# Kernel optimization log

Measured on AMD Instinct MI355X. Metric: run time of the kernel, lower is better.

Reference implementation:

```python
import jax, jax.numpy as jnp
import numpy as np

N = 4096
CIN = 128
COUT = 128
J = 2
SLOPE = 0.2        # LeakyReLU negative slope (GAT-style)
NEG = -9.0e15      # mask fill value from the source
ATT = J * COUT     # att_slice


def _leaky(v):
    return jnp.where(v >= 0, v, SLOPE * v)


def setup_inputs() -> dict:
    key = jax.random.key(0)
    ks = jax.random.split(key, 12)
    x = jax.random.normal(ks[0], (N, CIN), dtype=jnp.float32)

    def sparse_op(k):
        kv, km = jax.random.split(k)
        vals = jax.random.normal(kv, (N, N), dtype=jnp.float32)
        mask = jax.random.uniform(km, (N, N)) < 0.05
        return jnp.where(mask, vals, 0.0)

    Lu = sparse_op(ks[1])
    Ld = sparse_op(ks[2])
    P = jax.random.normal(ks[3], (N, N), dtype=jnp.float32) * 0.01  # harmonic projector

    s = 1.0 / np.sqrt(CIN)
    Wi_w = jax.random.uniform(ks[4], (J, CIN, COUT), minval=-s, maxval=s)
    Wi_b = jax.random.uniform(ks[5], (J, COUT), minval=-s, maxval=s)
    Ws_w = jax.random.uniform(ks[6], (J, CIN, COUT), minval=-s, maxval=s)
    Ws_b = jax.random.uniform(ks[7], (J, COUT), minval=-s, maxval=s)
    Wh_w = jax.random.uniform(ks[8], (CIN, COUT), minval=-s, maxval=s)
    Wh_b = jax.random.uniform(ks[9], (COUT,), minval=-s, maxval=s)
    att_irr = jax.random.normal(ks[10], (2 * ATT, 1), dtype=jnp.float32) * 0.1
    att_sol = jax.random.normal(ks[11], (2 * ATT, 1), dtype=jnp.float32) * 0.1
    return {"x": x, "Lu": Lu, "Ld": Ld, "P": P,
            "Wi_w": Wi_w, "Wi_b": Wi_b, "Ws_w": Ws_w, "Ws_b": Ws_b,
            "Wh_w": Wh_w, "Wh_b": Wh_b, "att_irr": att_irr, "att_sol": att_sol}


def reference(x, Lu, Ld, P, Wi_w, Wi_b, Ws_w, Ws_b, Wh_w, Wh_b, att_irr, att_sol):
    n = x.shape[0]
    # concat_j W_irr[j](x) -> [N, J*COUT] (j-major matches torch.cat along dim=1)
    x_irr = (jnp.einsum('nc,jco->njo', x, Wi_w) + Wi_b[None]).reshape(n, ATT)
    x_sol = (jnp.einsum('nc,jco->njo', x, Ws_w) + Ws_b[None]).reshape(n, ATT)

    # GAT-style scores: E[i,j] = leaky(s1[i] + s2[j])
    E_irr = _leaky(x_irr @ att_irr[:ATT] + (x_irr @ att_irr[ATT:]).T)
    E_sol = _leaky(x_sol @ att_sol[:ATT] + (x_sol @ att_sol[ATT:]).T)
    E_irr = jnp.where(Ld != 0, E_irr, NEG)
    E_sol = jnp.where(Lu != 0, E_sol, NEG)
    alpha_irr = jax.nn.softmax(E_irr, axis=1)  # dropout: eval mode -> identity
    alpha_sol = jax.nn.softmax(E_sol, axis=1)

    z = (alpha_irr @ x) @ Wi_w[0] + Wi_b[0] + (alpha_sol @ x) @ Ws_w[0] + Ws_b[0]
    for p in range(1, J):  # Laplacian-power aggregation
        alpha_irr = alpha_irr @ Ld
        alpha_sol = alpha_sol @ Lu
        z = z + (alpha_irr @ x) @ Wi_w[p] + Wi_b[p]
        z = z + (alpha_sol @ x) @ Ws_w[p] + Ws_b[p]
    z = z + (P @ x) @ Wh_w + Wh_b
    return z
```

## Files before the change

### kernel.cpp

```cpp
#include <hip/hip_runtime.h>

#define NN 4096
#define SLOPE 0.2f

typedef float f4_t __attribute__((ext_vector_type(4)));
typedef __bf16 bf8v __attribute__((ext_vector_type(8)));
typedef float f32x16 __attribute__((ext_vector_type(16)));

#define V_OFF     0
#define C_OFF     512
#define BT_OFF    516
#define S_OFF     1024
#define DEN_OFF   20480
#define HXI_OFF   32768
#define HXS_OFF   (HXI_OFF + NN*128)
#define UI_OFF    (HXS_OFF + NN*128)
#define US_OFF    (UI_OFF + NN*128)
#define XWH_OFF   (US_OFF + NN*128)
#define OI_OFF    (XWH_OFF + NN*128)
#define OS_OFF    (OI_OFF + NN*128)
#define ZP_OFF    (OS_OFF + NN*128)
#define WS_FLOATS (ZP_OFF + 8*NN*128)
#define XF_BYTE_OFF ((size_t)WS_FLOATS * 4)

#define XI(c)   ((c) + (((c) >> 5) << 2))

#define FRAG(c, k) ((size_t)((k) >> 4) * 2048 + (size_t)((c) >> 5) * 512 \
                    + (size_t)((((c) & 31) + 32 * (((k) >> 3) & 1)) * 8 + ((k) & 7)))

__device__ __forceinline__ unsigned short f2bf(float x) {
  unsigned u = __float_as_uint(x);
  return (unsigned short)((u + 0x7FFFu + ((u >> 16) & 1u)) >> 16);
}
__device__ __forceinline__ float bf2f(unsigned short h) {
  return __uint_as_float(((unsigned)h) << 16);
}
union BFU { unsigned short u[8]; bf8v v; };

__global__ __launch_bounds__(128) void k_prep(
    const float* __restrict__ Wi_w, const float* __restrict__ Wi_b,
    const float* __restrict__ Ws_w, const float* __restrict__ Ws_b,
    const float* __restrict__ Wh_b, const float* __restrict__ att_irr,
    const float* __restrict__ att_sol, float* __restrict__ ws) {
  const int t = threadIdx.x;
  float v1i = 0.f, v2i = 0.f, v1s = 0.f, v2s = 0.f;
  for (int j = 0; j < 2; ++j) {
    for (int o = 0; o < 128; ++o) {
      const float wi = Wi_w[j*16384 + t*128 + o];
      const float wv = Ws_w[j*16384 + t*128 + o];
      v1i += wi * att_irr[j*128 + o];
      v2i += wi * att_irr[256 + j*128 + o];
      v1s += wv * att_sol[j*128 + o];
      v2s += wv * att_sol[256 + j*128 + o];
    }
  }
  ws[V_OFF + t]       = v1i;
  ws[V_OFF + 128 + t] = v2i;
  ws[V_OFF + 256 + t] = v1s;
  ws[V_OFF + 384 + t] = v2s;
  ws[BT_OFF + t] = Wi_b[t] + Wi_b[128 + t] + Ws_b[t] + Ws_b[128 + t] + Wh_b[t];
  if (t < 4) {
    const float* bb = (t < 2) ? Wi_b : Ws_b;
    const float* aa = ((t < 2) ? att_irr : att_sol) + ((t & 1) ? 256 : 0);
    float c = 0.f;
    for (int k = 0; k < 256; ++k) c += bb[k] * aa[k];
    ws[C_OFF + t] = c;
  }
}

__global__ __launch_bounds__(256) void k_zero(float* __restrict__ ws) {
  const size_t q = ((size_t)blockIdx.x * 256 + threadIdx.x) * 4;
  if (q < (size_t)2*NN*128) {
    *(f4_t*)&ws[HXI_OFF + q] = (f4_t){0.f, 0.f, 0.f, 0.f};
  } else if (q < (size_t)4*NN*128) {
    *(f4_t*)&ws[OI_OFF + (q - (size_t)2*NN*128)] = (f4_t){0.f, 0.f, 0.f, 0.f};
  } else {
    const size_t r = q - (size_t)4*NN*128;
    if (r < 2*NN) *(f4_t*)&ws[DEN_OFF + r] = (f4_t){0.f, 0.f, 0.f, 0.f};
  }
}

__global__ __launch_bounds__(256) void k_pre2(
    const float* __restrict__ x, const float* __restrict__ Wh_w,
    float* __restrict__ ws, unsigned short* __restrict__ xth,
    unsigned short* __restrict__ xtl, unsigned short* __restrict__ xfh,
    unsigned short* __restrict__ xfl) {
  __shared__ __align__(16) float At[32][33];
  __shared__ __align__(16) float Wt[32][144];
  const int t = threadIdx.x;

  if (blockIdx.x < 128) {
    const int rb = blockIdx.x;
    const int rg = t >> 4, cg = t & 15;
    const int r0 = rb * 32;
    float acc[2][8];
    #pragma unroll
    for (int i = 0; i < 2; ++i)
      #pragma unroll
      for (int j = 0; j < 8; ++j) acc[i][j] = 0.f;
    for (int k0 = 0; k0 < 128; k0 += 32) {
      __syncthreads();
      {
        const int row = t >> 3, kq = t & 7;
        const float4 av = *(const float4*)&x[(r0 + row)*128 + k0 + kq*4];
        At[row][kq*4+0] = av.x; At[row][kq*4+1] = av.y;
        At[row][kq*4+2] = av.z; At[row][kq*4+3] = av.w;
      }
      #pragma unroll
      for (int l = 0; l < 4; ++l) {
        const int idx = t + l*256;
        const int kr = idx >> 5, c4 = idx & 31;
        const float4 wv = *(const float4*)&Wh_w[(k0 + kr)*128 + c4*4];
        *(float4*)&Wt[kr][XI(c4*4)] = wv;
      }
      __syncthreads();
      #pragma unroll
      for (int k = 0; k < 32; ++k) {
        const float a0 = At[rg*2 + 0][k];
        const float a1 = At[rg*2 + 1][k];
        const float4 b0 = *(const float4*)&Wt[k][XI(cg*8)];
        const float4 b1 = *(const float4*)&Wt[k][XI(cg*8 + 4)];
        acc[0][0] += a0*b0.x; acc[0][1] += a0*b0.y; acc[0][2] += a0*b0.z; acc[0][3] += a0*b0.w;
        acc[0][4] += a0*b1.x; acc[0][5] += a0*b1.y; acc[0][6] += a0*b1.z; acc[0][7] += a0*b1.w;
        acc[1][0] += a1*b0.x; acc[1][1] += a1*b0.y; acc[1][2] += a1*b0.z; acc[1][3] += a1*b0.w;
        acc[1][4] += a1*b1.x; acc[1][5] += a1*b1.y; acc[1][6] += a1*b1.z; acc[1][7] += a1*b1.w;
      }
    }
    #pragma unroll
    for (int i = 0; i < 2; ++i) {
      const int r = r0 + rg*2 + i;
      #pragma unroll
      for (int j = 0; j < 8; ++j) {
        const int c = cg*8 + j;
        const float val = acc[i][j];
        const unsigned short h = f2bf(val);
        const unsigned short l = f2bf(val - bf2f(h));
        const size_t fa = FRAG(c, r);
        xth[fa] = h;
        xtl[fa] = l;
      }
    }
  } else {
    const int wave = t >> 6, lane = t & 63;
    const int row = (blockIdx.x - 128) * 4 + wave;
    const float* v = ws + V_OFF;
    const float x0 = x[row*128 + lane];
    const float x1 = x[row*128 + 64 + lane];
    {
      const unsigned short h0 = f2bf(x0);
      const unsigned short l0 = f2bf(x0 - bf2f(h0));
      const size_t fa0 = FRAG(lane, row);
      xfh[fa0] = h0; xfl[fa0] = l0;
      const unsigned short h1 = f2bf(x1);
      const unsigned short l1 = f2bf(x1 - bf2f(h1));
      const size_t fa1 = FRAG(lane + 64, row);
      xfh[fa1] = h1; xfl[fa1] = l1;
    }
    float p0 = x0 * v[lane]       + x1 * v[64 + lane];
    float p1 = x0 * v[128 + lane] + x1 * v[192 + lane];
    float p2 = x0 * v[256 + lane] + x1 * v[320 + lane];
    float p3 = x0 * v[384 + lane] + x1 * v[448 + lane];
    #pragma unroll
    for (int off = 32; off; off >>= 1) {
      p0 += __shfl_down(p0, off);
      p1 += __shfl_down(p1, off);
      p2 += __shfl_down(p2, off);
      p3 += __shfl_down(p3, off);
    }
    if (lane == 0) {
      ws[S_OFF + row]          = p0 + ws[C_OFF + 0];
      ws[S_OFF + NN + row]     = p1 + ws[C_OFF + 1];
      ws[S_OFF + 2*NN + row]   = p2 + ws[C_OFF + 2];
      ws[S_OFF + 3*NN + row]   = p3 + ws[C_OFF + 3];
    }
  }
}

__global__ __launch_bounds__(256) void k_hxmm(
    const float* __restrict__ Ld, const float* __restrict__ Lu,
    const unsigned short* __restrict__ xfh, const unsigned short* __restrict__ xfl,
    float* __restrict__ ws) {
  const int bid = blockIdx.x;
  const int br  = (bid >> 2) & 1;
  const int idx = ((bid >> 3) << 2) | (bid & 3);
  const int rblk = idx & 127;
  const int kz   = idx >> 7;
  const int t = threadIdx.x;
  const int w = t >> 6, lane = t & 63;
  const int la = lane & 31, h = lane >> 5;
  const int r0 = rblk * 32;
  const int kc = kz * 1024;
  const float* __restrict__ L = br ? Lu : Ld;
  float* __restrict__ Hx = ws + (br ? HXS_OFF : HXI_OFF);

  __shared__ __align__(16) char buf[2][16384];

  f32x16 acc;
  #pragma unroll
  for (int e = 0; e < 16; ++e) acc[e] = 0.f;

  const int col4 = la;
  const unsigned short* __restrict__ bh0 = xfh + ((size_t)kc >> 4) * 2048 + w * 512 + lane * 8;
  const unsigned short* __restrict__ bl0 = xfl + ((size_t)kc >> 4) * 2048 + w * 512 + lane * 8;

  f4_t rv[4];
  #pragma unroll
  for (int i = 0; i < 4; ++i) {
    const int row = w*8 + i*2 + h;
    rv[i] = *(const f4_t*)&L[(size_t)(r0 + row) * NN + kc + col4 * 4];
  }

  for (int tt = 0; tt < 8; ++tt) {
    char* bd = buf[tt & 1];
    #pragma unroll
    for (int i = 0; i < 4; ++i) {
      const int row = w*8 + i*2 + h;
      *(f4_t*)(bd + row*512 + ((col4*16) ^ ((row & 15) << 4))) = rv[i];
    }
    __syncthreads();
    if (tt + 1 < 8) {
      const int kcol = kc + (tt + 1) * 128;
      #pragma unroll
      for (int i = 0; i < 4; ++i) {
        const int row = w*8 + i*2 + h;
        rv[i] = *(const f4_t*)&L[(size_t)(r0 + row) * NN + kcol + col4 * 4];
      }
    }
    const char* tb = buf[tt & 1];
    const int rowb = la * 512;
    const int mask = (la & 15) << 4;
    #pragma unroll
    for (int s = 0; s < 8; ++s) {
      const int k0 = s * 16;
      const int b0 = k0 * 4 + 32 * h;
      const f4_t a0 = *(const f4_t*)(tb + rowb + ((b0) ^ mask));
      const f4_t a1 = *(const f4_t*)(tb + rowb + ((b0 + 16) ^ mask));
      BFU ah, al;
      #pragma unroll
      for (int i = 0; i < 8; ++i) {
        const float f = (i < 4) ? a0[i] : a1[i - 4];
        const unsigned short hh = f2bf(f);
        ah.u[i] = hh;
        al.u[i] = f2bf(f - bf2f(hh));
      }
      const size_t bo = (size_t)(tt * 8 + s) * 2048;
      const bf8v bh = *(const bf8v*)(bh0 + bo);
      const bf8v bl = *(const bf8v*)(bl0 + bo);
      acc = __builtin_amdgcn_mfma_f32_32x32x16_bf16(ah.v, bh, acc, 0, 0, 0);
      acc = __builtin_amdgcn_mfma_f32_32x32x16_bf16(al.v, bh, acc, 0, 0, 0);
      acc = __builtin_amdgcn_mfma_f32_32x32x16_bf16(ah.v, bl, acc, 0, 0, 0);
    }
  }

  #pragma unroll
  for (int reg = 0; reg < 16; ++reg) {
    const int row = (reg & 3) + 8*(reg >> 2) + 4*h;
    atomicAdd(&Hx[(size_t)(r0 + row) * 128 + 32*w + la], acc[reg]);
  }
}

__global__ __launch_bounds__(256) void k_ugemm(
    const float* __restrict__ x, const float* __restrict__ Wi_w,
    const float* __restrict__ Ws_w, float* __restrict__ ws,
    unsigned short* __restrict__ uih, unsigned short* __restrict__ uil,
    unsigned short* __restrict__ ush, unsigned short* __restrict__ usl) {
  const int rb = blockIdx.x;
  const int sel = blockIdx.y;
  const float* A[2]; const float* W[2];
  unsigned short* uh; unsigned short* ul;
  if (sel == 0) { A[0]=x; W[0]=Wi_w; A[1]=ws+HXI_OFF; W[1]=Wi_w+16384; uh=uih; ul=uil; }
  else          { A[0]=x; W[0]=Ws_w; A[1]=ws+HXS_OFF; W[1]=Ws_w+16384; uh=ush; ul=usl; }

  __shared__ __align__(16) float At[32][33];
  __shared__ __align__(16) float Wt[32][144];
  const int t = threadIdx.x;
  const int rg = t >> 4, cg = t & 15;
  const int r0 = rb * 32;
  float acc[2][8];
  #pragma unroll
  for (int i = 0; i < 2; ++i)
    #pragma unroll
    for (int j = 0; j < 8; ++j) acc[i][j] = 0.f;

  for (int ps = 0; ps < 2; ++ps) {
    const float* __restrict__ Ap = A[ps];
    const float* __restrict__ Wp = W[ps];
    for (int k0 = 0; k0 < 128; k0 += 32) {
      __syncthreads();
      {
        const int row = t >> 3, kq = t & 7;
        const float4 av = *(const float4*)&Ap[(r0 + row)*128 + k0 + kq*4];
        At[row][kq*4+0] = av.x; At[row][kq*4+1] = av.y;
        At[row][kq*4+2] = av.z; At[row][kq*4+3] = av.w;
      }
      #pragma unroll
      for (int l = 0; l < 4; ++l) {
        const int idx = t + l*256;
        const int kr = idx >> 5, c4 = idx & 31;
        const float4 wv = *(const float4*)&Wp[(k0 + kr)*128 + c4*4];
        *(float4*)&Wt[kr][XI(c4*4)] = wv;
      }
      __syncthreads();
      #pragma unroll
      for (int k = 0; k < 32; ++k) {
        const float a0 = At[rg*2 + 0][k];
        const float a1 = At[rg*2 + 1][k];
        const float4 b0 = *(const float4*)&Wt[k][XI(cg*8)];
        const float4 b1 = *(const float4*)&Wt[k][XI(cg*8 + 4)];
        acc[0][0] += a0*b0.x; acc[0][1] += a0*b0.y; acc[0][2] += a0*b0.z; acc[0][3] += a0*b0.w;
        acc[0][4] += a0*b1.x; acc[0][5] += a0*b1.y; acc[0][6] += a0*b1.z; acc[0][7] += a0*b1.w;
        acc[1][0] += a1*b0.x; acc[1][1] += a1*b0.y; acc[1][2] += a1*b0.z; acc[1][3] += a1*b0.w;
        acc[1][4] += a1*b1.x; acc[1][5] += a1*b1.y; acc[1][6] += a1*b1.z; acc[1][7] += a1*b1.w;
      }
    }
  }
  #pragma unroll
  for (int i = 0; i < 2; ++i) {
    const int r = r0 + rg*2 + i;
    #pragma unroll
    for (int j = 0; j < 8; ++j) {
      const int c = cg*8 + j;
      const float val = acc[i][j];
      const unsigned short h = f2bf(val);
      const unsigned short l = f2bf(val - bf2f(h));
      const size_t fa = FRAG(c, r);
      uh[fa] = h;
      ul[fa] = l;
    }
  }
}

__global__ __launch_bounds__(256) void k_attnmm(
    const float* __restrict__ Ld, const float* __restrict__ Lu,
    float* __restrict__ ws, const unsigned short* __restrict__ uih,
    const unsigned short* __restrict__ uil, const unsigned short* __restrict__ ush,
    const unsigned short* __restrict__ usl) {
  const int bid = blockIdx.x;
  const int br  = (bid >> 2) & 1;
  const int idx = ((bid >> 3) << 2) | (bid & 3);
  const int rblk = idx & 127;
  const int kz   = idx >> 7;
  const int t = threadIdx.x;
  const int w = t >> 6, lane = t & 63;
  const int la = lane & 31, h = lane >> 5;
  const int r0 = rblk * 32;
  const int kc = kz * 1024;
  const float* __restrict__ L = br ? Lu : Ld;
  const unsigned short* __restrict__ ufh = br ? ush : uih;
  const unsigned short* __restrict__ ufl = br ? usl : uil;
  float* __restrict__ O = ws + (br ? OS_OFF : OI_OFF);
  float* __restrict__ den = ws + DEN_OFF + br * NN;
  const float s1v = ws[S_OFF + (br ? 2*NN : 0) + r0 + la];
  const float* __restrict__ s2b = ws + S_OFF + (br ? 3*NN : NN) + kc;

  __shared__ __align__(16) char buf[2][16384];

  f32x16 acc;
  #pragma unroll
  for (int e = 0; e < 16; ++e) acc[e] = 0.f;
  float dp = 0.f;

  const int col4 = la;
  const unsigned short* __restrict__ bh0 = ufh + ((size_t)kc >> 4) * 2048 + w * 512 + lane * 8;
  const unsigned short* __restrict__ bl0 = ufl + ((size_t)kc >> 4) * 2048 + w * 512 + lane * 8;

  f4_t rv[4];
  #pragma unroll
  for (int i = 0; i < 4; ++i) {
    const int row = w*8 + i*2 + h;
    rv[i] = *(const f4_t*)&L[(size_t)(r0 + row) * NN + kc + col4 * 4];
  }

  for (int tt = 0; tt < 8; ++tt) {
    char* bd = buf[tt & 1];
    #pragma unroll
    for (int i = 0; i < 4; ++i) {
      const int row = w*8 + i*2 + h;
      *(f4_t*)(bd + row*512 + ((col4*16) ^ ((row & 15) << 4))) = rv[i];
    }
    __syncthreads();
    if (tt + 1 < 8) {
      const int kcol = kc + (tt + 1) * 128;
      #pragma unroll
      for (int i = 0; i < 4; ++i) {
        const int row = w*8 + i*2 + h;
        rv[i] = *(const f4_t*)&L[(size_t)(r0 + row) * NN + kcol + col4 * 4];
      }
    }
    const char* tb = buf[tt & 1];
    const int rowb = la * 512;
    const int mask = (la & 15) << 4;
    #pragma unroll
    for (int s = 0; s < 8; ++s) {
      const int k0 = s * 16;
      const int b0 = k0 * 4 + 32 * h;
      const f4_t a0 = *(const f4_t*)(tb + rowb + ((b0) ^ mask));
      const f4_t a1 = *(const f4_t*)(tb + rowb + ((b0 + 16) ^ mask));
      const int kloc = tt * 128 + k0 + 8 * h;
      const f4_t s2a = *(const f4_t*)(s2b + kloc);
      const f4_t s2c = *(const f4_t*)(s2b + kloc + 4);
      BFU eh, el;
      #pragma unroll
      for (int i = 0; i < 8; ++i) {
        const float Lv = (i < 4) ? a0[i] : a1[i - 4];
        const float s2 = (i < 4) ? s2a[i] : s2c[i - 4];
        const float sc = s1v + s2;
        const float scl = sc >= 0.f ? sc : SLOPE * sc;
        const float ex = (Lv != 0.f) ? __expf(scl) : 0.f;
        dp += ex;
        const unsigned short hh = f2bf(ex);
        eh.u[i] = hh;
        el.u[i] = f2bf(ex - bf2f(hh));
      }
      const size_t bo = (size_t)(tt * 8 + s) * 2048;
      const bf8v bh = *(const bf8v*)(bh0 + bo);
      const bf8v bl = *(const bf8v*)(bl0 + bo);
      acc = __builtin_amdgcn_mfma_f32_32x32x16_bf16(eh.v, bh, acc, 0, 0, 0);
      acc = __builtin_amdgcn_mfma_f32_32x32x16_bf16(el.v, bh, acc, 0, 0, 0);
      acc = __builtin_amdgcn_mfma_f32_32x32x16_bf16(eh.v, bl, acc, 0, 0, 0);
    }
  }
  dp += __shfl_xor(dp, 32);
  if (w == 0 && lane < 32) atomicAdd(&den[r0 + la], dp);

  #pragma unroll
  for (int reg = 0; reg < 16; ++reg) {
    const int row = (reg & 3) + 8*(reg >> 2) + 4*h;
    atomicAdd(&O[(size_t)(r0 + row) * 128 + 32*w + la], acc[reg]);
  }
}

__global__ __launch_bounds__(256) void k_pgemm(
    const float* __restrict__ P, const unsigned short* __restrict__ xth,
    const unsigned short* __restrict__ xtl, float* __restrict__ zpart) {
  const int t = threadIdx.x;
  const int w = t >> 6, lane = t & 63;
  const int la = lane & 31;
  const int koff = (lane >> 5) * 8;
  const int r0 = blockIdx.x * 32;
  const int kz = blockIdx.y;
  const int kb = kz * 512 + w * 128;

  f32x16 acc[4];
  #pragma unroll
  for (int n = 0; n < 4; ++n)
    #pragma unroll
    for (int e = 0; e < 16; ++e) acc[n][e] = 0.f;

  const float* __restrict__ arow = P + (size_t)(r0 + la) * NN + kb + koff;
  const unsigned short* __restrict__ bh_base = xth + (size_t)kb * 128 + lane * 8;
  const unsigned short* __restrict__ bl_base = xtl + (size_t)kb * 128 + lane * 8;

  f4_t a0 = __builtin_nontemporal_load((const f4_t*)arow);
  f4_t a1 = __builtin_nontemporal_load((const f4_t*)(arow + 4));
  for (int s = 0; s < 8; ++s) {
    f4_t na0 = a0, na1 = a1;
    if (s < 7) {
      na0 = __builtin_nontemporal_load((const f4_t*)(arow + (s + 1) * 16));
      na1 = __builtin_nontemporal_load((const f4_t*)(arow + (s + 1) * 16 + 4));
    }
    BFU ah, al;
    #pragma unroll
    for (int i = 0; i < 8; ++i) {
      const float f = (i < 4) ? a0[i] : a1[i - 4];
      const unsigned short h = f2bf(f);
      ah.u[i] = h;
      al.u[i] = f2bf(f - bf2f(h));
    }
    const unsigned short* __restrict__ bh_s = bh_base + s * 2048;
    const unsigned short* __restrict__ bl_s = bl_base + s * 2048;
    #pragma unroll
    for (int n = 0; n < 4; ++n) {
      const bf8v bh = *(const bf8v*)(bh_s + n * 512);
      const bf8v bl = *(const bf8v*)(bl_s + n * 512);
      acc[n] = __builtin_amdgcn_mfma_f32_32x32x16_bf16(ah.v, bh, acc[n], 0, 0, 0);
      acc[n] = __builtin_amdgcn_mfma_f32_32x32x16_bf16(al.v, bh, acc[n], 0, 0, 0);
      acc[n] = __builtin_amdgcn_mfma_f32_32x32x16_bf16(ah.v, bl, acc[n], 0, 0, 0);
    }
    a0 = na0; a1 = na1;
  }

  __shared__ float red[2][32][128];
  if (w < 2) {
    #pragma unroll
    for (int n = 0; n < 4; ++n)
      #pragma unroll
      for (int reg = 0; reg < 16; ++reg) {
        const int row = (reg & 3) + 8*(reg >> 2) + 4*(lane >> 5);
        red[w][row][32*n + la] = acc[n][reg];
      }
  }
  __syncthreads();
  if (w >= 2) {
    #pragma unroll
    for (int n = 0; n < 4; ++n)
      #pragma unroll
      for (int reg = 0; reg < 16; ++reg) {
        const int row = (reg & 3) + 8*(reg >> 2) + 4*(lane >> 5);
        red[w - 2][row][32*n + la] += acc[n][reg];
      }
  }
  __syncthreads();
  float* __restrict__ zp = zpart + (size_t)kz * NN * 128;
  #pragma unroll
  for (int i = 0; i < 8; ++i) {
    const int row = w * 8 + i;
    zp[(size_t)(r0 + row) * 128 + lane]      = red[0][row][lane]      + red[1][row][lane];
    zp[(size_t)(r0 + row) * 128 + 64 + lane] = red[0][row][64 + lane] + red[1][row][64 + lane];
  }
}

__global__ __launch_bounds__(256) void k_combine(const float* __restrict__ ws,
                                                 float* __restrict__ z) {
  const int i = blockIdx.x * 256 + threadIdx.x;
  const int col = i & 127;
  const int row = i >> 7;
  const float di = ws[DEN_OFF + row];
  const float ds = ws[DEN_OFF + NN + row];
  float acc = ws[BT_OFF + col] + ws[OI_OFF + i] / di + ws[OS_OFF + i] / ds;
  #pragma unroll
  for (int kz = 0; kz < 8; ++kz) acc += ws[ZP_OFF + kz*NN*128 + i];
  z[i] = acc;
}

extern "C" void kernel_launch(void* const* d_in, const int* in_sizes, int n_in,
                              void* d_out, int out_size, void* d_ws, size_t ws_size,
                              hipStream_t stream) {
  const float* x       = (const float*)d_in[0];
  const float* Lu      = (const float*)d_in[1];
  const float* Ld      = (const float*)d_in[2];
  const float* P       = (const float*)d_in[3];
  const float* Wi_w    = (const float*)d_in[4];
  const float* Wi_b    = (const float*)d_in[5];
  const float* Ws_w    = (const float*)d_in[6];
  const float* Ws_b    = (const float*)d_in[7];
  const float* Wh_w    = (const float*)d_in[8];
  const float* Wh_b    = (const float*)d_in[9];
  const float* att_irr = (const float*)d_in[10];
  const float* att_sol = (const float*)d_in[11];
  float* z  = (float*)d_out;
  float* ws = (float*)d_ws;
  float*          zpart = ws + ZP_OFF;
  unsigned short* xth   = (unsigned short*)(ws + XWH_OFF);
  unsigned short* xtl   = xth + (size_t)128 * NN;
  unsigned short* uih   = (unsigned short*)(ws + UI_OFF);
  unsigned short* uil   = uih + (size_t)128 * NN;
  unsigned short* ush   = (unsigned short*)(ws + US_OFF);
  unsigned short* usl   = ush + (size_t)128 * NN;
  unsigned short* xfh   = (unsigned short*)((char*)d_ws + XF_BYTE_OFF);
  unsigned short* xfl   = xfh + (size_t)128 * NN;

  k_prep<<<1, 128, 0, stream>>>(Wi_w, Wi_b, Ws_w, Ws_b, Wh_b, att_irr, att_sol, ws);
  k_zero<<<(4*NN*128 + 2*NN) / 1024, 256, 0, stream>>>(ws);
  k_pre2<<<1152, 256, 0, stream>>>(x, Wh_w, ws, xth, xtl, xfh, xfl);
  k_hxmm<<<1024, 256, 0, stream>>>(Ld, Lu, xfh, xfl, ws);
  {
    dim3 g(128, 2);
    k_ugemm<<<g, 256, 0, stream>>>(x, Wi_w, Ws_w, ws, uih, uil, ush, usl);
  }
  k_attnmm<<<1024, 256, 0, stream>>>(Ld, Lu, ws, uih, uil, ush, usl);
  {
    dim3 g(128, 8);
    k_pgemm<<<g, 256, 0, stream>>>(P, xth, xtl, zpart);
  }
  k_combine<<<NN * 128 / 256, 256, 0, stream>>>(ws, z);
}
```

Baseline: 422.7 us.

## Convert L tiles to split-bf16 once at staging instead of per-wave

In k_hxmm and the attention GEMM kernel, the L tile (and in the attention kernel the masked exp scores) is now converted to hi/lo bf16 pairs once, when the tile is staged into shared memory, in MFMA fragment layout. Previously every wave re-read the fp32 tile and redid the conversion and exp for the same A fragment, so four waves duplicated that work. Waves now load ready-made bf16 fragments with a single vector read, and the conversion of the next tile overlaps with the current tile's MFMAs. The cost is a new swizzled LDS layout, a change in the row-sum reduction order for the denominator, and more live registers.

```diff
diff --git a/kernel.cpp b/kernel.cpp
--- a/kernel.cpp
+++ b/kernel.cpp
@@ -36,6 +36,7 @@
   return __uint_as_float(((unsigned)h) << 16);
 }
 union BFU { unsigned short u[8]; bf8v v; };
+union P8 { unsigned short u[4]; unsigned long long ull; };
 
 __global__ __launch_bounds__(128) void k_prep(
     const float* __restrict__ Wi_w, const float* __restrict__ Wi_b,
@@ -193,62 +194,82 @@
   const float* __restrict__ L = br ? Lu : Ld;
   float* __restrict__ Hx = ws + (br ? HXS_OFF : HXI_OFF);
 
-  __shared__ __align__(16) char buf[2][16384];
+  __shared__ __align__(16) char ahb[2][8192];
+  __shared__ __align__(16) char alb[2][8192];
 
   f32x16 acc;
   #pragma unroll
   for (int e = 0; e < 16; ++e) acc[e] = 0.f;
 
-  const int col4 = la;
+  const int s_t   = la >> 2;
+  const int xmask = s_t << 4;
+  const int j0b   = (la & 1) * 8;
+  const int lt_add = 32 * ((la >> 1) & 1);
+
   const unsigned short* __restrict__ bh0 = xfh + ((size_t)kc >> 4) * 2048 + w * 512 + lane * 8;
   const unsigned short* __restrict__ bl0 = xfl + ((size_t)kc >> 4) * 2048 + w * 512 + lane * 8;
 
-  f4_t rv[4];
+  f4_t rv[4], nv[4];
   #pragma unroll
   for (int i = 0; i < 4; ++i) {
     const int row = w*8 + i*2 + h;
-    rv[i] = *(const f4_t*)&L[(size_t)(r0 + row) * NN + kc + col4 * 4];
-  }
-
+    rv[i] = *(const f4_t*)&L[(size_t)(r0 + row) * NN + kc + la * 4];
+  }
+  #pragma unroll
+  for (int i = 0; i < 4; ++i) {
+    const int row = w*8 + i*2 + h;
+    const int off = s_t*1024 + (((row + lt_add)*16) ^ xmask) + j0b;
+    P8 ph, pl;
+    #pragma unroll
+    for (int c = 0; c < 4; ++c) {
+      const float f = rv[i][c];
+      const unsigned short hh = f2bf(f);
+      ph.u[c] = hh;
+      pl.u[c] = f2bf(f - bf2f(hh));
+    }
+    *(unsigned long long*)(ahb[0] + off) = ph.ull;
+    *(unsigned long long*)(alb[0] + off) = pl.ull;
+  }
+
+  #pragma unroll
   for (int tt = 0; tt < 8; ++tt) {
-    char* bd = buf[tt & 1];
-    #pragma unroll
-    for (int i = 0; i < 4; ++i) {
-      const int row = w*8 + i*2 + h;
-      *(f4_t*)(bd + row*512 + ((col4*16) ^ ((row & 15) << 4))) = rv[i];
-    }
-    __syncthreads();
-    if (tt + 1 < 8) {
-      const int kcol = kc + (tt + 1) * 128;
+    const int cur = tt & 1;
+    if (tt < 7) {
       #pragma unroll
       for (int i = 0; i < 4; ++i) {
         const int row = w*8 + i*2 + h;
-        rv[i] = *(const f4_t*)&L[(size_t)(r0 + row) * NN + kcol + col4 * 4];
-      }
-    }
-    const char* tb = buf[tt & 1];
-    const int rowb = la * 512;
-    const int mask = (la & 15) << 4;
+        nv[i] = *(const f4_t*)&L[(size_t)(r0 + row) * NN + kc + (tt+1)*128 + la * 4];
+      }
+    }
+    __syncthreads();
     #pragma unroll
     for (int s = 0; s < 8; ++s) {
-      const int k0 = s * 16;
-      const int b0 = k0 * 4 + 32 * h;
-      const f4_t a0 = *(const f4_t*)(tb + rowb + ((b0) ^ mask));
-      const f4_t a1 = *(const f4_t*)(tb + rowb + ((b0 + 16) ^ mask));
-      BFU ah, al;
-      #pragma unroll
-      for (int i = 0; i < 8; ++i) {
-        const float f = (i < 4) ? a0[i] : a1[i - 4];
-        const unsigned short hh = f2bf(f);
-        ah.u[i] = hh;
-        al.u[i] = f2bf(f - bf2f(hh));
-      }
+      const int ra = s*1024 + ((lane*16) ^ (s << 4));
+      const bf8v ah = *(const bf8v*)(ahb[cur] + ra);
+      const bf8v al = *(const bf8v*)(alb[cur] + ra);
       const size_t bo = (size_t)(tt * 8 + s) * 2048;
       const bf8v bh = *(const bf8v*)(bh0 + bo);
       const bf8v bl = *(const bf8v*)(bl0 + bo);
-      acc = __builtin_amdgcn_mfma_f32_32x32x16_bf16(ah.v, bh, acc, 0, 0, 0);
-      acc = __builtin_amdgcn_mfma_f32_32x32x16_bf16(al.v, bh, acc, 0, 0, 0);
-      acc = __builtin_amdgcn_mfma_f32_32x32x16_bf16(ah.v, bl, acc, 0, 0, 0);
+      acc = __builtin_amdgcn_mfma_f32_32x32x16_bf16(ah, bh, acc, 0, 0, 0);
+      acc = __builtin_amdgcn_mfma_f32_32x32x16_bf16(al, bh, acc, 0, 0, 0);
+      acc = __builtin_amdgcn_mfma_f32_32x32x16_bf16(ah, bl, acc, 0, 0, 0);
+    }
+    if (tt < 7) {
+      #pragma unroll
+      for (int i = 0; i < 4; ++i) {
+        const int row = w*8 + i*2 + h;
+        const int off = s_t*1024 + (((row + lt_add)*16) ^ xmask) + j0b;
+        P8 ph, pl;
+        #pragma unroll
+        for (int c = 0; c < 4; ++c) {
+          const float f = nv[i][c];
+          const unsigned short hh = f2bf(f);
+          ph.u[c] = hh;
+          pl.u[c] = f2bf(f - bf2f(hh));
+        }
+        *(unsigned long long*)(ahb[cur ^ 1] + off) = ph.ull;
+        *(unsigned long long*)(alb[cur ^ 1] + off) = pl.ull;
+      }
     }
   }
 
@@ -350,78 +371,113 @@
   const unsigned short* __restrict__ ufl = br ? usl : uil;
   float* __restrict__ O = ws + (br ? OS_OFF : OI_OFF);
   float* __restrict__ den = ws + DEN_OFF + br * NN;
-  const float s1v = ws[S_OFF + (br ? 2*NN : 0) + r0 + la];
+  const float* __restrict__ s1b = ws + S_OFF + (br ? 2*NN : 0) + r0;
   const float* __restrict__ s2b = ws + S_OFF + (br ? 3*NN : NN) + kc;
 
-  __shared__ __align__(16) char buf[2][16384];
+  __shared__ __align__(16) char ahb[2][8192];
+  __shared__ __align__(16) char alb[2][8192];
 
   f32x16 acc;
   #pragma unroll
   for (int e = 0; e < 16; ++e) acc[e] = 0.f;
-  float dp = 0.f;
-
-  const int col4 = la;
+  float dp[4] = {0.f, 0.f, 0.f, 0.f};
+
+  const int s_t   = la >> 2;
+  const int xmask = s_t << 4;
+  const int j0b   = (la & 1) * 8;
+  const int lt_add = 32 * ((la >> 1) & 1);
+
+  float s1r[4];
+  #pragma unroll
+  for (int i = 0; i < 4; ++i) s1r[i] = s1b[w*8 + i*2 + h];
+
   const unsigned short* __restrict__ bh0 = ufh + ((size_t)kc >> 4) * 2048 + w * 512 + lane * 8;
   const unsigned short* __restrict__ bl0 = ufl + ((size_t)kc >> 4) * 2048 + w * 512 + lane * 8;
 
-  f4_t rv[4];
+  f4_t rv[4], nv[4];
   #pragma unroll
   for (int i = 0; i < 4; ++i) {
     const int row = w*8 + i*2 + h;
-    rv[i] = *(const f4_t*)&L[(size_t)(r0 + row) * NN + kc + col4 * 4];
-  }
-
-  for (int tt = 0; tt < 8; ++tt) {
-    char* bd = buf[tt & 1];
+    rv[i] = *(const f4_t*)&L[(size_t)(r0 + row) * NN + kc + la * 4];
+  }
+  {
+    const f4_t s2v = *(const f4_t*)(s2b + la * 4);
     #pragma unroll
     for (int i = 0; i < 4; ++i) {
       const int row = w*8 + i*2 + h;
-      *(f4_t*)(bd + row*512 + ((col4*16) ^ ((row & 15) << 4))) = rv[i];
-    }
-    __syncthreads();
-    if (tt + 1 < 8) {
-      const int kcol = kc + (tt + 1) * 128;
+      const int off = s_t*1024 + (((row + lt_add)*16) ^ xmask) + j0b;
+      P8 ph, pl;
+      #pragma unroll
+      for (int c = 0; c < 4; ++c) {
+        const float sc = s1r[i] + s2v[c];
+        const float scl = sc >= 0.f ? sc : SLOPE * sc;
+        const float ex = (rv[i][c] != 0.f) ? __expf(scl) : 0.f;
+        dp[i] += ex;
+        const unsigned short hh = f2bf(ex);
+        ph.u[c] = hh;
+        pl.u[c] = f2bf(ex - bf2f(hh));
+      }
+      *(unsigned long long*)(ahb[0] + off) = ph.ull;
+      *(unsigned long long*)(alb[0] + off) = pl.ull;
+    }
+  }
+
+  #pragma unroll
+  for (int tt = 0; tt < 8; ++tt) {
+    const int cur = tt & 1;
+    if (tt < 7) {
       #pragma unroll
       for (int i = 0; i < 4; ++i) {
         const int row = w*8 + i*2 + h;
-        rv[i] = *(const f4_t*)&L[(size_t)(r0 + row) * NN + kcol + col4 * 4];
-      }
-    }
-    const char* tb = buf[tt & 1];
-    const int rowb = la * 512;
-    const int mask = (la & 15) << 4;
+        nv[i] = *(const f4_t*)&L[(size_t)(r0 + row) * NN + kc + (tt+1)*128 + la * 4];
+      }
+    }
+    __syncthreads();
     #pragma unroll
     for (int s = 0; s < 8; ++s) {
-      const int k0 = s * 16;
-      const int b0 = k0 * 4 + 32 * h;
-      const f4_t a0 = *(const f4_t*)(tb + rowb + ((b0) ^ mask));
-      const f4_t a1 = *(const f4_t*)(tb + rowb + ((b0 + 16) ^ mask));
-      const int kloc = tt * 128 + k0 + 8 * h;
-      const f4_t s2a = *(const f4_t*)(s2b + kloc);
-      const f4_t s2c = *(const f4_t*)(s2b + kloc + 4);
-      BFU eh, el;
-      #pragma unroll
-      for (int i = 0; i < 8; ++i) {
-        const float Lv = (i < 4) ? a0[i] : a1[i - 4];
-        const float s2 = (i < 4) ? s2a[i] : s2c[i - 4];
-        const float sc = s1v + s2;
-        const float scl = sc >= 0.f ? sc : SLOPE * sc;
-        const float ex = (Lv != 0.f) ? __expf(scl) : 0.f;
-        dp += ex;
-        const unsigned short hh = f2bf(ex);
-        eh.u[i] = hh;
-        el.u[i] = f2bf(ex - bf2f(hh));
-      }
+      const int ra = s*1024 + ((lane*16) ^ (s << 4));
+      const bf8v ah = *(const bf8v*)(ahb[cur] + ra);
+      const bf8v al = *(const bf8v*)(alb[cur] + ra);
       const size_t bo = (size_t)(tt * 8 + s) * 2048;
       const bf8v bh = *(const bf8v*)(bh0 + bo);
       const bf8v bl = *(const bf8v*)(bl0 + bo);
-      acc = __builtin_amdgcn_mfma_f32_32x32x16_bf16(eh.v, bh, acc, 0, 0, 0);
-      acc = __builtin_amdgcn_mfma_f32_32x32x16_bf16(el.v, bh, acc, 0, 0, 0);
-      acc = __builtin_amdgcn_mfma_f32_32x32x16_bf16(eh.v, bl, acc, 0, 0, 0);
-    }
-  }
-  dp += __shfl_xor(dp, 32);
-  if (w == 0 && lane < 32) atomicAdd(&den[r0 + la], dp);
+      acc = __builtin_amdgcn_mfma_f32_32x32x16_bf16(ah, bh, acc, 0, 0, 0);
+      acc = __builtin_amdgcn_mfma_f32_32x32x16_bf16(al, bh, acc, 0, 0, 0);
+      acc = __builtin_amdgcn_mfma_f32_32x32x16_bf16(ah, bl, acc, 0, 0, 0);
+    }
+    if (tt < 7) {
+      const f4_t s2v = *(const f4_t*)(s2b + (tt+1)*128 + la * 4);
+      #pragma unroll
+      for (int i = 0; i < 4; ++i) {
+        const int row = w*8 + i*2 + h;
+        const int off = s_t*1024 + (((row + lt_add)*16) ^ xmask) + j0b;
+        P8 ph, pl;
+        #pragma unroll
+        for (int c = 0; c < 4; ++c) {
+          const float sc = s1r[i] + s2v[c];
+          const float scl = sc >= 0.f ? sc : SLOPE * sc;
+          const float ex = (nv[i][c] != 0.f) ? __expf(scl) : 0.f;
+          dp[i] += ex;
+          const unsigned short hh = f2bf(ex);
+          ph.u[c] = hh;
+          pl.u[c] = f2bf(ex - bf2f(hh));
+        }
+        *(unsigned long long*)(ahb[cur ^ 1] + off) = ph.ull;
+        *(unsigned long long*)(alb[cur ^ 1] + off) = pl.ull;
+      }
+    }
+  }
+
+  #pragma unroll
+  for (int i = 0; i < 4; ++i) {
+    #pragma unroll
+    for (int off = 16; off; off >>= 1) dp[i] += __shfl_xor(dp[i], off);
+  }
+  if (la == 0) {
+    #pragma unroll
+    for (int i = 0; i < 4; ++i)
+      atomicAdd(&den[r0 + w*8 + i*2 + h], dp[i]);
+  }
 
   #pragma unroll
   for (int reg = 0; reg < 16; ++reg) {
```

After: 394.9 us. 1.07x faster.
